# Optimization experiments

Measured on AMD Instinct MI355X. Metric: run time of the kernel, lower is better.

Reference implementation:

```python
import jax, jax.numpy as jnp
import numpy as np

DIM, E, K, H = 512, 8, 2, 16  # hidden_dim is hardcoded to 16 in the torch module
B, N = 8, 4096
BN_EPS = 1e-5


def setup_inputs() -> dict:
    key = jax.random.key(0)
    ks = jax.random.split(key, 12)
    s = 0.02
    return {
        "x": jax.random.normal(ks[0], (B, N, DIM), jnp.float32),
        # gate: Conv1d(dim, dim, 1) -> weight [dim, dim]; BatchNorm1d(dim); Conv1d(dim, E, 1)
        "wg1": jax.random.normal(ks[1], (DIM, DIM), jnp.float32) * s,
        "bg1": jnp.zeros((DIM,), jnp.float32),
        "gamma": jnp.ones((DIM,), jnp.float32),
        "beta": jnp.zeros((DIM,), jnp.float32),
        "wg2": jax.random.normal(ks[2], (E, DIM), jnp.float32) * s,
        "bg2": jnp.zeros((E,), jnp.float32),
        # experts stacked: Linear(dim,16) -> w1 [E, dim, 16]; Linear(16,dim) -> w2 [E, 16, dim]
        "w1": jax.random.normal(ks[3], (E, DIM, H), jnp.float32) * s,
        "b1": jnp.zeros((E, H), jnp.float32),
        "w2": jax.random.normal(ks[4], (E, H, DIM), jnp.float32) * s,
        "b2": jnp.zeros((E, DIM), jnp.float32),
    }


def reference(x, wg1, bg1, gamma, beta, wg2, bg2, w1, b1, w2, b2):
    b, n, c = x.shape
    t = b * n
    flat = x.reshape(t, c)                                 # [T, C]

    # gate: 1x1 conv == per-token linear; BN over all tokens per channel (train-mode batch stats)
    h = flat @ wg1.T + bg1                                  # [T, C]
    mu = h.mean(axis=0)
    var = h.var(axis=0)                                     # biased, matches torch BN normalization
    h = gamma * (h - mu) * jax.lax.rsqrt(var + BN_EPS) + beta
    h = jax.nn.relu(h)
    logits = h @ wg2.T + bg2                                # [T, E]

    vals, idx = jax.lax.top_k(logits, K)                    # [T, K]
    topk_w = jax.nn.softmax(vals, axis=-1)
    weight = jnp.zeros((t, logits.shape[-1]), logits.dtype)
    weight = weight.at[jnp.arange(t)[:, None], idx].set(topk_w)  # scatter, [T, E]

    # dense expert compute for every token (faithful to original)
    h1 = jax.nn.relu(jnp.einsum('tc,ech->teh', flat, w1) + b1)   # [T, E, H]
    all_out = jnp.einsum('teh,ehc->tec', h1, w2) + b2            # [T, E, C]
    out_flat = jnp.einsum('tec,te->tc', all_out, weight)         # masked combine

    out = out_flat.reshape(b, n, c).transpose(0, 2, 1)           # [B, C, N]
    usage = weight.sum(axis=0) / t
    lb_loss = (usage ** 2).sum() * logits.shape[-1]
    return out, lb_loss
```

## Files before the change

### kernel.cpp

```cpp
#include <hip/hip_runtime.h>

#define T_TOK 32768
#define C_DIM 512
#define N_SEQ 4096

typedef unsigned short ushort_t;
typedef unsigned int uint_t;
typedef __attribute__((ext_vector_type(8))) _Float16 half8;
typedef __attribute__((ext_vector_type(4))) float f32x4;

static __device__ __forceinline__ ushort_t f2h_bits(float f) {
  _Float16 h = (_Float16)f;
  return __builtin_bit_cast(ushort_t, h);
}
static __device__ __forceinline__ float h_bits2f(ushort_t u) {
  return (float)__builtin_bit_cast(_Float16, u);
}

static __device__ __forceinline__ half8 frag_ld(const ushort_t* base, int r, int q) {
  const int off = r * 32 + ((q ^ ((r >> 1) & 3)) * 8);
  return *(const half8*)(base + off);
}

#define GLOAD_LDS(gptr, lptr)                                                  \
  __builtin_amdgcn_global_load_lds(                                            \
      (const __attribute__((address_space(1))) uint_t*)(gptr),                 \
      (__attribute__((address_space(3))) uint_t*)(lptr), 16, 0, 0)

__global__ __launch_bounds__(256) void prep(
    const float* __restrict__ X, const float* __restrict__ wg1,
    const float* __restrict__ w1, const float* __restrict__ w2,
    const float* __restrict__ b2, ushort_t* __restrict__ Ahi,
    ushort_t* __restrict__ Alo, ushort_t* __restrict__ Whi,
    ushort_t* __restrict__ Wlo, ushort_t* __restrict__ W1t,
    ushort_t* __restrict__ W2t, float* __restrict__ stats,
    float* __restrict__ usage, uint_t* __restrict__ done) {
  const int idx = blockIdx.x * 256 + threadIdx.x;
  {
    const size_t i0 = (size_t)idx * 8;
    float4 a = *(const float4*)(X + i0);
    float4 b = *(const float4*)(X + i0 + 4);
    float v[8] = {a.x, a.y, a.z, a.w, b.x, b.y, b.z, b.w};
    ushort_t hi[8], lo[8];
#pragma unroll
    for (int j = 0; j < 8; ++j) {
      hi[j] = f2h_bits(v[j]);
      lo[j] = f2h_bits(v[j] - h_bits2f(hi[j]));
    }
    *(uint4*)(Ahi + i0) = *(uint4*)hi;
    *(uint4*)(Alo + i0) = *(uint4*)lo;
  }
  if (blockIdx.x < 1024) {
    {
      const float v = wg1[idx];
      const ushort_t h = f2h_bits(v);
      Whi[idx] = h;
      Wlo[idx] = f2h_bits(v - h_bits2f(h));
    }
    if (idx < 65536) {
      const int eh = idx >> 9, c = idx & 511;
      const int e = eh >> 4, hh = eh & 15;
      W1t[idx] = f2h_bits(w1[((size_t)e * 512 + c) * 16 + hh]);
    }
    if (idx < 81920) {
      const int c = idx / 160, k = idx - c * 160;
      float v = 0.f;
      if (k < 128) {
        const int e = k >> 4, hh = k & 15;
        v = w2[((size_t)e * 16 + hh) * 512 + c];
      } else if (k < 136) {
        v = b2[(size_t)(k - 128) * 512 + c];
      }
      W2t[c * 160 + k] = f2h_bits(v);
    }
  }
  if (blockIdx.x == 4096) {
    float4 z = {0.f, 0.f, 0.f, 0.f};
    *(float4*)&stats[threadIdx.x * 4] = z;
    if (threadIdx.x < 8) usage[threadIdx.x] = 0.f;
    if (threadIdx.x == 8) *done = 0u;
  }
}

__global__ __launch_bounds__(256) void k1_mfma(
    const ushort_t* __restrict__ Ahi, const ushort_t* __restrict__ Alo,
    const ushort_t* __restrict__ Whi, const ushort_t* __restrict__ Wlo,
    const float* __restrict__ bg1, float* __restrict__ H,
    float* __restrict__ stats) {
  __shared__ ushort_t sAh[4096], sAl[4096], sBh[4096], sBl[4096];
  const int tid = threadIdx.x, lane = tid & 63, w = tid >> 6;
  const int wm = w >> 1, wn = w & 1;
  const int b = blockIdx.x;
  const int m0 = ((b & 7) | ((b >> 5) << 3)) * 128;
  const int n0 = ((b >> 3) & 3) * 128;

  const ushort_t* gsrc;
  ushort_t* lbase;
  int rowbase;
  if (w == 0)      { gsrc = Ahi; lbase = sAh; rowbase = m0; }
  else if (w == 1) { gsrc = Alo; lbase = sAl; rowbase = m0; }
  else if (w == 2) { gsrc = Whi; lbase = sBh; rowbase = n0; }
  else             { gsrc = Wlo; lbase = sBl; rowbase = n0; }

  f32x4 acc[4][4] = {};
  const int cl = lane & 15, qf = lane >> 4;

  for (int kc = 0; kc < 16; ++kc) {
    const int k0 = kc * 32;
    __syncthreads();
#pragma unroll
    for (int j = 0; j < 8; ++j) {
      const int p = j * 64 + lane;
      const int r = p >> 2, q = (p & 3) ^ ((r >> 1) & 3);
      GLOAD_LDS(gsrc + (size_t)(rowbase + r) * 512 + k0 + q * 8, lbase + j * 512);
    }
    __syncthreads();
    half8 ah[4], al[4], bh[4], bl[4];
#pragma unroll
    for (int f = 0; f < 4; ++f) {
      ah[f] = frag_ld(sAh, wm * 64 + f * 16 + cl, qf);
      al[f] = frag_ld(sAl, wm * 64 + f * 16 + cl, qf);
      bh[f] = frag_ld(sBh, wn * 64 + f * 16 + cl, qf);
      bl[f] = frag_ld(sBl, wn * 64 + f * 16 + cl, qf);
    }
#pragma unroll
    for (int i = 0; i < 4; ++i)
#pragma unroll
      for (int j = 0; j < 4; ++j) {
        acc[i][j] = __builtin_amdgcn_mfma_f32_16x16x32_f16(ah[i], bh[j], acc[i][j], 0, 0, 0);
        acc[i][j] = __builtin_amdgcn_mfma_f32_16x16x32_f16(ah[i], bl[j], acc[i][j], 0, 0, 0);
        acc[i][j] = __builtin_amdgcn_mfma_f32_16x16x32_f16(al[i], bh[j], acc[i][j], 0, 0, 0);
      }
  }

  float s[4] = {0, 0, 0, 0}, qs[4] = {0, 0, 0, 0};
  const int rq = lane >> 4;
#pragma unroll
  for (int nf = 0; nf < 4; ++nf) {
    const int col = n0 + wn * 64 + nf * 16 + cl;
    const float bv = bg1[col];
#pragma unroll
    for (int mf = 0; mf < 4; ++mf) {
      const int row = m0 + wm * 64 + mf * 16 + rq * 4;
#pragma unroll
      for (int i = 0; i < 4; ++i) {
        const float v = acc[mf][nf][i] + bv;
        H[(size_t)(row + i) * 512 + col] = v;
        s[nf] += v;
        qs[nf] += v * v;
      }
    }
  }
#pragma unroll
  for (int nf = 0; nf < 4; ++nf) {
    s[nf] += __shfl_xor(s[nf], 16, 64);
    qs[nf] += __shfl_xor(qs[nf], 16, 64);
    s[nf] += __shfl_xor(s[nf], 32, 64);
    qs[nf] += __shfl_xor(qs[nf], 32, 64);
  }
  if (lane < 16) {
#pragma unroll
    for (int nf = 0; nf < 4; ++nf) {
      const int col = n0 + wn * 64 + nf * 16 + cl;
      atomicAdd(&stats[col], s[nf]);
      atomicAdd(&stats[512 + col], qs[nf]);
    }
  }
}

__global__ __launch_bounds__(256) void k5_fused(
    const ushort_t* __restrict__ Ahi, const ushort_t* __restrict__ W1t,
    const ushort_t* __restrict__ W2t, const float* __restrict__ b1,
    const float* __restrict__ H, const float* __restrict__ stats,
    const float* __restrict__ gamma, const float* __restrict__ beta,
    const float* __restrict__ wg2, const float* __restrict__ bg2,
    float* __restrict__ usage, uint_t* __restrict__ done,
    float* __restrict__ Out) {
  __shared__ ushort_t sA[2048], sB[4096];
  __shared__ ushort_t Pl[64 * 168];
  __shared__ float wtab[64 * 8];
  __shared__ float ys[128 * 68];
  __shared__ float scsh_l[1024];
  __shared__ float lus[8];

  const int tid = threadIdx.x, lane = tid & 63, w = tid >> 6;
  const int wm = w >> 1, wn = w & 1;
  const int t0 = blockIdx.x * 64;
  const int bi = t0 >> 12, n0 = t0 & 4095;
  const int cl = lane & 15, qf = lane >> 4, rq = lane >> 4;

  if (tid < 8) lus[tid] = 0.f;
  wtab[tid] = 0.f;
  wtab[tid + 256] = 0.f;
  {
    uint4 z = {0, 0, 0, 0};
    const int row = tid >> 2, hf = tid & 3;
    *(uint4*)&Pl[row * 168 + 128 + hf * 8] = z;
  }
#pragma unroll
  for (int rep = 0; rep < 2; ++rep) {
    const int c = tid + rep * 256;
    const double mu = (double)stats[c] * (1.0 / (double)T_TOK);
    const double var = (double)stats[512 + c] * (1.0 / (double)T_TOK) - mu * mu;
    const double rstd = 1.0 / sqrt(var + 1e-5);
    const float scv = (float)((double)gamma[c] * rstd);
    scsh_l[c] = scv;
    scsh_l[512 + c] = beta[c] - (float)mu * scv;
  }
  __syncthreads();

  {
    const int cb = lane * 8;
    float sc[8], sh[8];
#pragma unroll
    for (int i = 0; i < 8; ++i) {
      sc[i] = scsh_l[cb + i];
      sh[i] = scsh_l[512 + cb + i];
    }
    float wg[8][8];
#pragma unroll
    for (int e = 0; e < 8; ++e)
#pragma unroll
      for (int i = 0; i < 8; ++i) wg[e][i] = wg2[e * C_DIM + cb + i];
    float bg[8];
#pragma unroll
    for (int e = 0; e < 8; ++e) bg[e] = bg2[e];

#pragma unroll 2
    for (int it = 0; it < 16; ++it) {
      const int tl = w * 16 + it;
      const float* hr = H + (size_t)(t0 + tl) * C_DIM + cb;
      float4 h0 = *(const float4*)hr;
      float4 h1 = *(const float4*)(hr + 4);
      float y[8] = {h0.x, h0.y, h0.z, h0.w, h1.x, h1.y, h1.z, h1.w};
#pragma unroll
      for (int i = 0; i < 8; ++i) y[i] = fmaxf(fmaf(y[i], sc[i], sh[i]), 0.f);

      float lg[8];
#pragma unroll
      for (int e = 0; e < 8; ++e) {
        float sum = 0.f;
#pragma unroll
        for (int i = 0; i < 8; ++i) sum = fmaf(y[i], wg[e][i], sum);
        lg[e] = sum;
      }
#pragma unroll
      for (int d = 1; d < 64; d <<= 1)
#pragma unroll
        for (int e = 0; e < 8; ++e) lg[e] += __shfl_xor(lg[e], d, 64);
#pragma unroll
      for (int e = 0; e < 8; ++e) lg[e] += bg[e];

      float v1 = lg[0]; int i1 = 0;
#pragma unroll
      for (int e = 1; e < 8; ++e)
        if (lg[e] > v1) { v1 = lg[e]; i1 = e; }
      float v2 = -3.4e38f; int i2 = 0;
#pragma unroll
      for (int e = 0; e < 8; ++e)
        if (e != i1 && lg[e] > v2) { v2 = lg[e]; i2 = e; }

      const float p = expf(v2 - v1);
      const float rw = 1.f / (1.f + p);
      const float w0 = rw, w1 = p * rw;

      if (lane == 0) {
        wtab[tl * 8 + i1] = w0;
        wtab[tl * 8 + i2] = w1;
        Pl[tl * 168 + 128 + i1] = f2h_bits(w0);
        Pl[tl * 168 + 128 + i2] = f2h_bits(w1);
        atomicAdd(&lus[i1], w0);
        atomicAdd(&lus[i2], w1);
      }
    }
  }
  __syncthreads();
  if (tid < 8) atomicAdd(&usage[tid], lus[tid]);
  __syncthreads();
  if (tid == 0) {
    __threadfence();
    const uint_t ticket = atomicAdd(done, 1u);
    if (ticket == 511u) {
      float s = 0.f;
#pragma unroll
      for (int e = 0; e < 8; ++e) {
        const float u = atomicAdd(&usage[e], 0.f) * (1.f / (float)T_TOK);
        s += u * u;
      }
      Out[(size_t)16777216] = s * 8.f;
    }
  }

  f32x4 acc[2][4] = {};
  for (int kc = 0; kc < 16; ++kc) {
    const int k0 = kc * 32;
    __syncthreads();
#pragma unroll
    for (int j = 0; j < 3; ++j) {
      const int p0 = w * 192 + j * 64;
      const int p = p0 + lane;
      if (p0 < 256) {
        const int r = p >> 2, q = (p & 3) ^ ((r >> 1) & 3);
        GLOAD_LDS(Ahi + (size_t)(t0 + r) * 512 + k0 + q * 8, sA + p0 * 8);
      } else {
        const int pb = p - 256;
        const int r = pb >> 2, q = (pb & 3) ^ ((r >> 1) & 3);
        GLOAD_LDS(W1t + (size_t)r * 512 + k0 + q * 8, sB + (p0 - 256) * 8);
      }
    }
    __syncthreads();
    half8 af[2], bf[4];
#pragma unroll
    for (int f = 0; f < 2; ++f) af[f] = frag_ld(sA, wm * 32 + f * 16 + cl, qf);
#pragma unroll
    for (int f = 0; f < 4; ++f) bf[f] = frag_ld(sB, wn * 64 + f * 16 + cl, qf);
#pragma unroll
    for (int i = 0; i < 2; ++i)
#pragma unroll
      for (int j = 0; j < 4; ++j)
        acc[i][j] = __builtin_amdgcn_mfma_f32_16x16x32_f16(af[i], bf[j], acc[i][j], 0, 0, 0);
  }

  {
#pragma unroll
    for (int nf = 0; nf < 4; ++nf) {
      const int col = wn * 64 + nf * 16 + cl;
      const float bv = b1[col];
      const int e = wn * 4 + nf;
#pragma unroll
      for (int mf = 0; mf < 2; ++mf) {
        const int row = wm * 32 + mf * 16 + rq * 4;
#pragma unroll
        for (int i = 0; i < 4; ++i) {
          const float v = fmaxf(acc[mf][nf][i] + bv, 0.f) * wtab[(row + i) * 8 + e];
          Pl[(row + i) * 168 + col] = f2h_bits(v);
        }
      }
    }
  }

  for (int nc = 0; nc < 4; ++nc) {
    f32x4 a2[2][4] = {};
    for (int kc = 0; kc < 5; ++kc) {
      const int k0 = kc * 32;
      __syncthreads();
#pragma unroll
      for (int j = 0; j < 2; ++j) {
        const int p0 = w * 128 + j * 64;
        const int pb = p0 + lane;
        const int r = pb >> 2, q = (pb & 3) ^ ((r >> 1) & 3);
        GLOAD_LDS(W2t + (size_t)(nc * 128 + r) * 160 + k0 + q * 8, sB + p0 * 8);
      }
      __syncthreads();
      half8 af[2], bf4[4];
#pragma unroll
      for (int f = 0; f < 2; ++f)
        af[f] = *(const half8*)(Pl + (wm * 32 + f * 16 + cl) * 168 + k0 + qf * 8);
#pragma unroll
      for (int f = 0; f < 4; ++f) bf4[f] = frag_ld(sB, wn * 64 + f * 16 + cl, qf);
#pragma unroll
      for (int i = 0; i < 2; ++i)
#pragma unroll
        for (int j = 0; j < 4; ++j)
          a2[i][j] = __builtin_amdgcn_mfma_f32_16x16x32_f16(af[i], bf4[j], a2[i][j], 0, 0, 0);
    }
    __syncthreads();
#pragma unroll
    for (int nf = 0; nf < 4; ++nf) {
      const int c = wn * 64 + nf * 16 + cl;
#pragma unroll
      for (int mf = 0; mf < 2; ++mf) {
        const int trow = wm * 32 + mf * 16 + rq * 4;
#pragma unroll
        for (int i = 0; i < 4; ++i) ys[c * 68 + trow + i] = a2[mf][nf][i];
      }
    }
    __syncthreads();
#pragma unroll
    for (int pass = 0; pass < 8; ++pass) {
      const int c = pass * 16 + (tid >> 4);
      const int f4 = tid & 15;
      float4 v = *(const float4*)&ys[c * 68 + f4 * 4];
      *(float4*)&Out[((size_t)(bi * 512 + nc * 128 + c)) * 4096 + n0 + f4 * 4] = v;
    }
  }
}

extern "C" void kernel_launch(void* const* d_in, const int* in_sizes, int n_in,
                              void* d_out, int out_size, void* d_ws, size_t ws_size,
                              hipStream_t stream) {
  const float* x     = (const float*)d_in[0];
  const float* wg1   = (const float*)d_in[1];
  const float* bg1   = (const float*)d_in[2];
  const float* gamma = (const float*)d_in[3];
  const float* beta  = (const float*)d_in[4];
  const float* wg2   = (const float*)d_in[5];
  const float* bg2   = (const float*)d_in[6];
  const float* w1    = (const float*)d_in[7];
  const float* b1    = (const float*)d_in[8];
  const float* w2    = (const float*)d_in[9];
  const float* b2    = (const float*)d_in[10];
  float* out = (float*)d_out;

  char* ws = (char*)d_ws;
  float*    h     = (float*)ws;
  ushort_t* Ahi   = (ushort_t*)(ws + 67108864);
  ushort_t* Alo   = (ushort_t*)(ws + 100663296);
  ushort_t* Whi   = (ushort_t*)(ws + 134217728);
  ushort_t* Wlo   = (ushort_t*)(ws + 134742016);
  ushort_t* W1t   = (ushort_t*)(ws + 135266304);
  ushort_t* W2t   = (ushort_t*)(ws + 135397376);
  float*    stats = (float*)(ws + 135561216);
  float*    usage = (float*)(ws + 135565312);
  uint_t*   done  = (uint_t*)(ws + 135565344);

  prep<<<8192, 256, 0, stream>>>(x, wg1, w1, w2, b2, Ahi, Alo, Whi, Wlo, W1t,
                                 W2t, stats, usage, done);
  k1_mfma<<<1024, 256, 0, stream>>>(Ahi, Alo, Whi, Wlo, bg1, h, stats);
  k5_fused<<<512, 256, 0, stream>>>(Ahi, W1t, W2t, b1, h, stats, gamma, beta,
                                    wg2, bg2, usage, done, out);
}
```

Before: 265.2 us.

## Double-buffer activation tiles in LDS and load weight fragments directly from global

In both the gate GEMM and the fused expert kernel, activation tiles now go into double-buffered LDS. The next K-chunk is prefetched while the current one is consumed, which leaves one barrier per iteration. Weight fragments (Whi/Wlo, W1t, W2t) are read straight from global/L2 into registers instead of being staged through LDS, which cuts LDS traffic and barriers. The trade-off is uncoalesced, L2-dependent global loads in the inner loop. There is also a possible race: the loop's only barrier sits before the async prefetch into the other buffer, so a fast wave may overwrite data others are still reading.

```diff
diff --git a/kernel.cpp b/kernel.cpp
--- a/kernel.cpp
+++ b/kernel.cpp
@@ -87,41 +87,49 @@
     const ushort_t* __restrict__ Whi, const ushort_t* __restrict__ Wlo,
     const float* __restrict__ bg1, float* __restrict__ H,
     float* __restrict__ stats) {
-  __shared__ ushort_t sAh[4096], sAl[4096], sBh[4096], sBl[4096];
+  __shared__ ushort_t sAh[2][4096], sAl[2][4096];
   const int tid = threadIdx.x, lane = tid & 63, w = tid >> 6;
   const int wm = w >> 1, wn = w & 1;
   const int b = blockIdx.x;
   const int m0 = ((b & 7) | ((b >> 5) << 3)) * 128;
   const int n0 = ((b >> 3) & 3) * 128;
-
-  const ushort_t* gsrc;
-  ushort_t* lbase;
-  int rowbase;
-  if (w == 0)      { gsrc = Ahi; lbase = sAh; rowbase = m0; }
-  else if (w == 1) { gsrc = Alo; lbase = sAl; rowbase = m0; }
-  else if (w == 2) { gsrc = Whi; lbase = sBh; rowbase = n0; }
-  else             { gsrc = Wlo; lbase = sBl; rowbase = n0; }
+  const int cl = lane & 15, qf = lane >> 4;
+
+  const ushort_t* gA = (w < 2) ? Ahi : Alo;
+
+#define K1_STAGE(kc, buf)                                                      \
+  {                                                                            \
+    const int k0s = (kc) * 32;                                                 \
+    ushort_t* lb = (w < 2) ? sAh[buf] : sAl[buf];                              \
+    _Pragma("unroll") for (int j = 0; j < 4; ++j) {                            \
+      const int p = j * 128 + (w & 1) * 64 + lane;                             \
+      const int r = p >> 2, q = (p & 3) ^ ((r >> 1) & 3);                      \
+      GLOAD_LDS(gA + (size_t)(m0 + r) * 512 + k0s + q * 8, lb + p * 8);        \
+    }                                                                          \
+  }
 
   f32x4 acc[4][4] = {};
-  const int cl = lane & 15, qf = lane >> 4;
+  K1_STAGE(0, 0);
 
   for (int kc = 0; kc < 16; ++kc) {
     const int k0 = kc * 32;
     __syncthreads();
-#pragma unroll
-    for (int j = 0; j < 8; ++j) {
-      const int p = j * 64 + lane;
-      const int r = p >> 2, q = (p & 3) ^ ((r >> 1) & 3);
-      GLOAD_LDS(gsrc + (size_t)(rowbase + r) * 512 + k0 + q * 8, lbase + j * 512);
-    }
-    __syncthreads();
-    half8 ah[4], al[4], bh[4], bl[4];
+    if (kc < 15) K1_STAGE(kc + 1, (kc + 1) & 1);
+
+    half8 bh[4], bl[4];
 #pragma unroll
     for (int f = 0; f < 4; ++f) {
-      ah[f] = frag_ld(sAh, wm * 64 + f * 16 + cl, qf);
-      al[f] = frag_ld(sAl, wm * 64 + f * 16 + cl, qf);
-      bh[f] = frag_ld(sBh, wn * 64 + f * 16 + cl, qf);
-      bl[f] = frag_ld(sBl, wn * 64 + f * 16 + cl, qf);
+      const size_t r = (size_t)(n0 + wn * 64 + f * 16 + cl);
+      bh[f] = *(const half8*)(Whi + r * 512 + k0 + qf * 8);
+      bl[f] = *(const half8*)(Wlo + r * 512 + k0 + qf * 8);
+    }
+    half8 ah[4], al[4];
+    const ushort_t* bAh = sAh[kc & 1];
+    const ushort_t* bAl = sAl[kc & 1];
+#pragma unroll
+    for (int f = 0; f < 4; ++f) {
+      ah[f] = frag_ld(bAh, wm * 64 + f * 16 + cl, qf);
+      al[f] = frag_ld(bAl, wm * 64 + f * 16 + cl, qf);
     }
 #pragma unroll
     for (int i = 0; i < 4; ++i)
@@ -132,6 +140,7 @@
         acc[i][j] = __builtin_amdgcn_mfma_f32_16x16x32_f16(al[i], bh[j], acc[i][j], 0, 0, 0);
       }
   }
+#undef K1_STAGE
 
   float s[4] = {0, 0, 0, 0}, qs[4] = {0, 0, 0, 0};
   const int rq = lane >> 4;
@@ -176,7 +185,7 @@
     const float* __restrict__ wg2, const float* __restrict__ bg2,
     float* __restrict__ usage, uint_t* __restrict__ done,
     float* __restrict__ Out) {
-  __shared__ ushort_t sA[2048], sB[4096];
+  __shared__ ushort_t sA[2][2048];
   __shared__ ushort_t Pl[64 * 168];
   __shared__ float wtab[64 * 8];
   __shared__ float ys[128 * 68];
@@ -188,6 +197,12 @@
   const int t0 = blockIdx.x * 64;
   const int bi = t0 >> 12, n0 = t0 & 4095;
   const int cl = lane & 15, qf = lane >> 4, rq = lane >> 4;
+
+  {
+    const int p = tid;
+    const int r = p >> 2, q = (p & 3) ^ ((r >> 1) & 3);
+    GLOAD_LDS(Ahi + (size_t)(t0 + r) * 512 + q * 8, sA[0] + p * 8);
+  }
 
   if (tid < 8) lus[tid] = 0.f;
   wtab[tid] = 0.f;
@@ -295,25 +310,19 @@
   for (int kc = 0; kc < 16; ++kc) {
     const int k0 = kc * 32;
     __syncthreads();
-#pragma unroll
-    for (int j = 0; j < 3; ++j) {
-      const int p0 = w * 192 + j * 64;
-      const int p = p0 + lane;
-      if (p0 < 256) {
-        const int r = p >> 2, q = (p & 3) ^ ((r >> 1) & 3);
-        GLOAD_LDS(Ahi + (size_t)(t0 + r) * 512 + k0 + q * 8, sA + p0 * 8);
-      } else {
-        const int pb = p - 256;
-        const int r = pb >> 2, q = (pb & 3) ^ ((r >> 1) & 3);
-        GLOAD_LDS(W1t + (size_t)r * 512 + k0 + q * 8, sB + (p0 - 256) * 8);
-      }
-    }
-    __syncthreads();
-    half8 af[2], bf[4];
-#pragma unroll
-    for (int f = 0; f < 2; ++f) af[f] = frag_ld(sA, wm * 32 + f * 16 + cl, qf);
-#pragma unroll
-    for (int f = 0; f < 4; ++f) bf[f] = frag_ld(sB, wn * 64 + f * 16 + cl, qf);
+    if (kc < 15) {
+      const int p = tid;
+      const int r = p >> 2, q = (p & 3) ^ ((r >> 1) & 3);
+      GLOAD_LDS(Ahi + (size_t)(t0 + r) * 512 + (k0 + 32) + q * 8,
+                sA[(kc + 1) & 1] + p * 8);
+    }
+    half8 bf[4];
+#pragma unroll
+    for (int f = 0; f < 4; ++f)
+      bf[f] = *(const half8*)(W1t + (size_t)(wn * 64 + f * 16 + cl) * 512 + k0 + qf * 8);
+    half8 af[2];
+#pragma unroll
+    for (int f = 0; f < 2; ++f) af[f] = frag_ld(sA[kc & 1], wm * 32 + f * 16 + cl, qf);
 #pragma unroll
     for (int i = 0; i < 2; ++i)
 #pragma unroll
@@ -338,26 +347,21 @@
       }
     }
   }
+  __syncthreads();
 
   for (int nc = 0; nc < 4; ++nc) {
     f32x4 a2[2][4] = {};
+#pragma unroll
     for (int kc = 0; kc < 5; ++kc) {
       const int k0 = kc * 32;
-      __syncthreads();
-#pragma unroll
-      for (int j = 0; j < 2; ++j) {
-        const int p0 = w * 128 + j * 64;
-        const int pb = p0 + lane;
-        const int r = pb >> 2, q = (pb & 3) ^ ((r >> 1) & 3);
-        GLOAD_LDS(W2t + (size_t)(nc * 128 + r) * 160 + k0 + q * 8, sB + p0 * 8);
-      }
-      __syncthreads();
-      half8 af[2], bf4[4];
+      half8 bf4[4];
+#pragma unroll
+      for (int f = 0; f < 4; ++f)
+        bf4[f] = *(const half8*)(W2t + (size_t)(nc * 128 + wn * 64 + f * 16 + cl) * 160 + k0 + qf * 8);
+      half8 af[2];
 #pragma unroll
       for (int f = 0; f < 2; ++f)
         af[f] = *(const half8*)(Pl + (wm * 32 + f * 16 + cl) * 168 + k0 + qf * 8);
-#pragma unroll
-      for (int f = 0; f < 4; ++f) bf4[f] = frag_ld(sB, wn * 64 + f * 16 + cl, qf);
 #pragma unroll
       for (int i = 0; i < 2; ++i)
 #pragma unroll
```

After: 288.4 us. 1.09x slower.

## Halve k5 token tile, double-buffer A, read expert weights directly from global

Applied to the files above, without the earlier changes.

The fused expert kernel now processes 32 tokens per block instead of 64 and launches 1024 blocks, which should give more parallelism and lower LDS use per block. The A tile is double-buffered with an async prefetch of the next K chunk, and the W1/W2 fragments are loaded straight from global memory (L2-resident) instead of being staged through LDS. This removes several barriers per K step but reloads the weights once per block, so weight traffic doubles. The loss-finalization ticket threshold is updated to match the new block count.

```diff
diff --git a/kernel.cpp b/kernel.cpp
--- a/kernel.cpp
+++ b/kernel.cpp
@@ -176,23 +176,28 @@
     const float* __restrict__ wg2, const float* __restrict__ bg2,
     float* __restrict__ usage, uint_t* __restrict__ done,
     float* __restrict__ Out) {
-  __shared__ ushort_t sA[2048], sB[4096];
-  __shared__ ushort_t Pl[64 * 168];
-  __shared__ float wtab[64 * 8];
-  __shared__ float ys[128 * 68];
+  __shared__ ushort_t sA[2][1024];
+  __shared__ ushort_t Pl[32 * 168];
+  __shared__ float wtab[32 * 8];
+  __shared__ float ys[128 * 36];
   __shared__ float scsh_l[1024];
   __shared__ float lus[8];
 
   const int tid = threadIdx.x, lane = tid & 63, w = tid >> 6;
   const int wm = w >> 1, wn = w & 1;
-  const int t0 = blockIdx.x * 64;
+  const int t0 = blockIdx.x * 32;
   const int bi = t0 >> 12, n0 = t0 & 4095;
   const int cl = lane & 15, qf = lane >> 4, rq = lane >> 4;
 
+  if (tid < 128) {
+    const int p = tid;
+    const int r = p >> 2, q = (p & 3) ^ ((r >> 1) & 3);
+    GLOAD_LDS(Ahi + (size_t)(t0 + r) * 512 + q * 8, sA[0] + p * 8);
+  }
+
   if (tid < 8) lus[tid] = 0.f;
-  wtab[tid] = 0.f;
-  wtab[tid + 256] = 0.f;
-  {
+  if (tid < 256) wtab[tid] = 0.f;
+  if (tid < 128) {
     uint4 z = {0, 0, 0, 0};
     const int row = tid >> 2, hf = tid & 3;
     *(uint4*)&Pl[row * 168 + 128 + hf * 8] = z;
@@ -227,8 +232,8 @@
     for (int e = 0; e < 8; ++e) bg[e] = bg2[e];
 
 #pragma unroll 2
-    for (int it = 0; it < 16; ++it) {
-      const int tl = w * 16 + it;
+    for (int it = 0; it < 8; ++it) {
+      const int tl = w * 8 + it;
       const float* hr = H + (size_t)(t0 + tl) * C_DIM + cb;
       float4 h0 = *(const float4*)hr;
       float4 h1 = *(const float4*)(hr + 4);
@@ -280,7 +285,7 @@
   if (tid == 0) {
     __threadfence();
     const uint_t ticket = atomicAdd(done, 1u);
-    if (ticket == 511u) {
+    if (ticket == 1023u) {
       float s = 0.f;
 #pragma unroll
       for (int e = 0; e < 8; ++e) {
@@ -291,34 +296,24 @@
     }
   }
 
-  f32x4 acc[2][4] = {};
+  f32x4 acc4[4] = {};
   for (int kc = 0; kc < 16; ++kc) {
     const int k0 = kc * 32;
     __syncthreads();
-#pragma unroll
-    for (int j = 0; j < 3; ++j) {
-      const int p0 = w * 192 + j * 64;
-      const int p = p0 + lane;
-      if (p0 < 256) {
-        const int r = p >> 2, q = (p & 3) ^ ((r >> 1) & 3);
-        GLOAD_LDS(Ahi + (size_t)(t0 + r) * 512 + k0 + q * 8, sA + p0 * 8);
-      } else {
-        const int pb = p - 256;
-        const int r = pb >> 2, q = (pb & 3) ^ ((r >> 1) & 3);
-        GLOAD_LDS(W1t + (size_t)r * 512 + k0 + q * 8, sB + (p0 - 256) * 8);
-      }
-    }
-    __syncthreads();
-    half8 af[2], bf[4];
-#pragma unroll
-    for (int f = 0; f < 2; ++f) af[f] = frag_ld(sA, wm * 32 + f * 16 + cl, qf);
-#pragma unroll
-    for (int f = 0; f < 4; ++f) bf[f] = frag_ld(sB, wn * 64 + f * 16 + cl, qf);
-#pragma unroll
-    for (int i = 0; i < 2; ++i)
-#pragma unroll
-      for (int j = 0; j < 4; ++j)
-        acc[i][j] = __builtin_amdgcn_mfma_f32_16x16x32_f16(af[i], bf[j], acc[i][j], 0, 0, 0);
+    if (kc < 15 && tid < 128) {
+      const int p = tid;
+      const int r = p >> 2, q = (p & 3) ^ ((r >> 1) & 3);
+      GLOAD_LDS(Ahi + (size_t)(t0 + r) * 512 + (k0 + 32) + q * 8,
+                sA[(kc + 1) & 1] + p * 8);
+    }
+    half8 bf[4];
+#pragma unroll
+    for (int f = 0; f < 4; ++f)
+      bf[f] = *(const half8*)(W1t + (size_t)(wn * 64 + f * 16 + cl) * 512 + k0 + qf * 8);
+    half8 af = frag_ld(sA[kc & 1], wm * 16 + cl, qf);
+#pragma unroll
+    for (int j = 0; j < 4; ++j)
+      acc4[j] = __builtin_amdgcn_mfma_f32_16x16x32_f16(af, bf[j], acc4[j], 0, 0, 0);
   }
 
   {
@@ -327,60 +322,44 @@
       const int col = wn * 64 + nf * 16 + cl;
       const float bv = b1[col];
       const int e = wn * 4 + nf;
-#pragma unroll
-      for (int mf = 0; mf < 2; ++mf) {
-        const int row = wm * 32 + mf * 16 + rq * 4;
-#pragma unroll
-        for (int i = 0; i < 4; ++i) {
-          const float v = fmaxf(acc[mf][nf][i] + bv, 0.f) * wtab[(row + i) * 8 + e];
-          Pl[(row + i) * 168 + col] = f2h_bits(v);
-        }
-      }
-    }
-  }
+      const int row = wm * 16 + rq * 4;
+#pragma unroll
+      for (int i = 0; i < 4; ++i) {
+        const float v = fmaxf(acc4[nf][i] + bv, 0.f) * wtab[(row + i) * 8 + e];
+        Pl[(row + i) * 168 + col] = f2h_bits(v);
+      }
+    }
+  }
+  __syncthreads();
 
   for (int nc = 0; nc < 4; ++nc) {
-    f32x4 a2[2][4] = {};
+    f32x4 a2[4] = {};
+#pragma unroll
     for (int kc = 0; kc < 5; ++kc) {
       const int k0 = kc * 32;
-      __syncthreads();
-#pragma unroll
-      for (int j = 0; j < 2; ++j) {
-        const int p0 = w * 128 + j * 64;
-        const int pb = p0 + lane;
-        const int r = pb >> 2, q = (pb & 3) ^ ((r >> 1) & 3);
-        GLOAD_LDS(W2t + (size_t)(nc * 128 + r) * 160 + k0 + q * 8, sB + p0 * 8);
-      }
-      __syncthreads();
-      half8 af[2], bf4[4];
-#pragma unroll
-      for (int f = 0; f < 2; ++f)
-        af[f] = *(const half8*)(Pl + (wm * 32 + f * 16 + cl) * 168 + k0 + qf * 8);
-#pragma unroll
-      for (int f = 0; f < 4; ++f) bf4[f] = frag_ld(sB, wn * 64 + f * 16 + cl, qf);
-#pragma unroll
-      for (int i = 0; i < 2; ++i)
-#pragma unroll
-        for (int j = 0; j < 4; ++j)
-          a2[i][j] = __builtin_amdgcn_mfma_f32_16x16x32_f16(af[i], bf4[j], a2[i][j], 0, 0, 0);
+      half8 bf4[4];
+#pragma unroll
+      for (int f = 0; f < 4; ++f)
+        bf4[f] = *(const half8*)(W2t + (size_t)(nc * 128 + wn * 64 + f * 16 + cl) * 160 + k0 + qf * 8);
+      half8 af = *(const half8*)(Pl + (wm * 16 + cl) * 168 + k0 + qf * 8);
+#pragma unroll
+      for (int j = 0; j < 4; ++j)
+        a2[j] = __builtin_amdgcn_mfma_f32_16x16x32_f16(af, bf4[j], a2[j], 0, 0, 0);
     }
     __syncthreads();
 #pragma unroll
     for (int nf = 0; nf < 4; ++nf) {
       const int c = wn * 64 + nf * 16 + cl;
-#pragma unroll
-      for (int mf = 0; mf < 2; ++mf) {
-        const int trow = wm * 32 + mf * 16 + rq * 4;
-#pragma unroll
-        for (int i = 0; i < 4; ++i) ys[c * 68 + trow + i] = a2[mf][nf][i];
-      }
+      const int trow = wm * 16 + rq * 4;
+#pragma unroll
+      for (int i = 0; i < 4; ++i) ys[c * 36 + trow + i] = a2[nf][i];
     }
     __syncthreads();
 #pragma unroll
-    for (int pass = 0; pass < 8; ++pass) {
-      const int c = pass * 16 + (tid >> 4);
-      const int f4 = tid & 15;
-      float4 v = *(const float4*)&ys[c * 68 + f4 * 4];
+    for (int pass = 0; pass < 4; ++pass) {
+      const int c = pass * 32 + (tid >> 3);
+      const int f4 = tid & 7;
+      float4 v = *(const float4*)&ys[c * 36 + f4 * 4];
       *(float4*)&Out[((size_t)(bi * 512 + nc * 128 + c)) * 4096 + n0 + f4 * 4] = v;
     }
   }
@@ -417,6 +396,6 @@
   prep<<<8192, 256, 0, stream>>>(x, wg1, w1, w2, b2, Ahi, Alo, Whi, Wlo, W1t,
                                  W2t, stats, usage, done);
   k1_mfma<<<1024, 256, 0, stream>>>(Ahi, Alo, Whi, Wlo, bg1, h, stats);
-  k5_fused<<<512, 256, 0, stream>>>(Ahi, W1t, W2t, b1, h, stats, gamma, beta,
-                                    wg2, bg2, usage, done, out);
-}
+  k5_fused<<<1024, 256, 0, stream>>>(Ahi, W1t, W2t, b1, h, stats, gamma, beta,
+                                     wg2, bg2, usage, done, out);
+}
```

After: 303.3 us. +14.4%, slower.
